# Kernel optimization log

Measured on AMD Instinct MI355X. Metric: run time of the kernel, lower is better.

Reference implementation:

```python
import jax, jax.numpy as jnp
import numpy as np

B, P, J, MOT, K, NB, WN, H = 64, 12273, 80, 94, 64, 20, 17, 128
W_POSE = 1.0

def euler_to_rotmat(a):
    # a: [..., 3] radians, R = Rz @ Ry @ Rx
    sx, sy, sz = jnp.sin(a[..., 0]), jnp.sin(a[..., 1]), jnp.sin(a[..., 2])
    cx, cy, cz = jnp.cos(a[..., 0]), jnp.cos(a[..., 1]), jnp.cos(a[..., 2])
    r00 = cz * cy; r01 = cz * sy * sx - sz * cx; r02 = cz * sy * cx + sz * sx
    r10 = sz * cy; r11 = sz * sy * sx + cz * cx; r12 = sz * sy * cx - cz * sx
    r20 = -sy;     r21 = cy * sx;                r22 = cy * cx
    return jnp.stack([jnp.stack([r00, r01, r02], -1),
                      jnp.stack([r10, r11, r12], -1),
                      jnp.stack([r20, r21, r22], -1)], -2)

def setup_inputs() -> dict:
    key = jax.random.key(0)
    ks = jax.random.split(key, 20)
    f32 = jnp.float32
    return {
        'in_pc_batch': jax.random.normal(ks[0], (B, P, 3), f32),
        't_nor': jax.random.normal(ks[1], (B, P, 3), f32),
        'rest_verts': jax.random.normal(ks[2], (P, 3), f32),
        'skin_weights': jax.random.uniform(ks[3], (P, J), f32),
        'mul_weight_list': jax.random.normal(ks[4], (J, MOT), f32),
        'query': jax.random.normal(ks[5], (B, J, 3), f32),
        'cloth_pose_std': jax.random.uniform(ks[6], (3,), f32),
        'cloth_pose_mean': jax.random.normal(ks[7], (3,), f32),
        'cloth_trans_std': jax.random.uniform(ks[8], (3,), f32),
        'cloth_trans_mean': jax.random.normal(ks[9], (3,), f32),
        'W1': jax.random.normal(ks[10], (3 + K, H), f32) * 0.1,
        'b1': jnp.zeros((H,), f32),
        'W2': jax.random.normal(ks[11], (H, 6), f32) * 0.1,
        'b2': jnp.zeros((6,), f32),
        'tmtemp': jax.random.normal(ks[12], (B, MOT, K), f32),
        'Wd': jax.random.normal(ks[13], (MOT * K, NB * WN), f32) * 0.02,
        'bd': jnp.zeros((NB * WN,), f32),
        'DPSD': jax.random.normal(ks[14], (NB, WN, P, 3), f32) * 0.1,
        'ssdr_res_std': jax.random.uniform(ks[15], (3,), f32),
        'ssdr_res_mean': jax.random.normal(ks[16], (3,), f32),
    }

def reference(in_pc_batch, t_nor, rest_verts, skin_weights, mul_weight_list,
              query, cloth_pose_std, cloth_pose_mean, cloth_trans_std,
              cloth_trans_mean, W1, b1, W2, b2, tmtemp, Wd, bd, DPSD,
              ssdr_res_std, ssdr_res_mean):
    # per-joint field input: [B, J, K]
    field_input = jnp.einsum('bjk,lj->blk', tmtemp, jax.nn.relu(mul_weight_list))
    # FieldNet: per-joint MLP on concat(query, field_input) -> [B, J, 6]
    h = jnp.concatenate([query, field_input], axis=-1)
    pred_rt = jax.nn.relu(h @ W1 + b1) @ W2 + b2
    pred_pose = pred_rt[..., 0:3] * cloth_pose_std + cloth_pose_mean
    pred_trans = (query + pred_rt[..., 3:6]) * cloth_trans_std + cloth_trans_mean
    # detailsnet + fused 20-basis accumulation: [B, P, 3]
    nbat = tmtemp.shape[0]
    detailkey = (tmtemp.reshape(nbat, -1) @ Wd + bd).reshape(nbat, NB, WN)
    detail_res = jnp.einsum('bnw,nwpx->bpx', detailkey, DPSD)
    detail_res = detail_res * ssdr_res_std + ssdr_res_mean
    # SSDR LBS skinning with Euler-angle rotations (degrees -> radians)
    R = euler_to_rotmat(jnp.deg2rad(pred_pose))            # [B, J, 3, 3]
    skinned = (jnp.einsum('pj,bjxy,py->bpx', skin_weights, R, rest_verts)
               + jnp.einsum('pj,bjx->bpx', skin_weights, pred_trans))
    out_pc = skinned + detail_res                          # [B, P, 3]
    loss_pose_l1 = jnp.mean(jnp.abs(in_pc_batch[:, :, 0:3] - out_pc))
    loss = loss_pose_l1 * W_POSE + 1e-4 * jnp.mean(DPSD ** 2)
    return loss[None], out_pc
```

## Files before the change

kernel.cpp:

```cpp
#include <hip/hip_runtime.h>

#define B_   64
#define P_   12273
#define J_   80
#define MOT_ 94
#define K_   64
#define H_   128
#define Q_   340
#define NE_  36819
#define MK_  6016
#define PW_  12288
#define STG_ 2356416

typedef float v4f  __attribute__((ext_vector_type(4)));
typedef float v8f  __attribute__((ext_vector_type(8)));
typedef float v16f __attribute__((ext_vector_type(16)));
#define AS4 __attribute__((address_space(4)))

__device__ __forceinline__ const AS4 float* unif(const float* p){
  return (const AS4 float*)(unsigned long long)p;
}
__device__ __forceinline__ const AS4 v4f* univ4(const float* p){
  return (const AS4 v4f*)(unsigned long long)p;
}
__device__ __forceinline__ const AS4 v16f* univ16(const float* p){
  return (const AS4 v16f*)(unsigned long long)p;
}

__global__ __launch_bounds__(256) void k_prep(
    const float* __restrict__ query, const float* __restrict__ mwl,
    const float* __restrict__ tm,    const float* __restrict__ W1,
    const float* __restrict__ b1,    const float* __restrict__ W2,
    const float* __restrict__ b2,    const float* __restrict__ cps,
    const float* __restrict__ cpm,   const float* __restrict__ cts,
    const float* __restrict__ ctm,   const float* __restrict__ skin,
    float* __restrict__ G,           float* __restrict__ tm_t,
    float* __restrict__ w_t,         float* __restrict__ lacc)
{
  __shared__ float smem[80 * 65];
  int blk = blockIdx.x;
  int t = threadIdx.x;
  if (blk < 1280){
    int lane = t & 63;
    int wid = __builtin_amdgcn_readfirstlane(t >> 6);
    int bj = blk * 4 + wid;
    int b = bj / J_, l = bj - b * J_;
    float* hs = smem + wid * 80;
    float acc = 0.f;
    const AS4 float* mp = unif(mwl + l * MOT_);
    const float* tp = tm + (size_t)b * MK_ + lane;
    float tbuf[4];
    #pragma unroll
    for (int s = 0; s < 4; s++) tbuf[s] = tp[s * K_];
    #pragma unroll 4
    for (int j = 0; j < MOT_; j++){
      float tv = tbuf[j & 3];
      if (j + 4 < MOT_) tbuf[j & 3] = tp[(j + 4) * K_];
      float w = mp[j]; w = w > 0.f ? w : 0.f;
      acc = fmaf(w, tv, acc);
    }
    hs[3 + lane] = acc;
    if (lane < 3) hs[lane] = query[(size_t)bj * 3 + lane];
    __syncthreads();
    float a1 = b1[lane], a2 = b1[lane + 64];
    float wa[4], wb[4];
    #pragma unroll
    for (int s = 0; s < 4; s++){
      wa[s] = W1[s * H_ + lane];
      wb[s] = W1[s * H_ + 64 + lane];
    }
    #pragma unroll 4
    for (int i = 0; i < 67; i++){
      float hv = hs[i];
      float va = wa[i & 3], vb = wb[i & 3];
      if (i + 4 < 67){
        wa[i & 3] = W1[(i + 4) * H_ + lane];
        wb[i & 3] = W1[(i + 4) * H_ + 64 + lane];
      }
      a1 = fmaf(hv, va, a1);
      a2 = fmaf(hv, vb, a2);
    }
    a1 = a1 > 0.f ? a1 : 0.f;
    a2 = a2 > 0.f ? a2 : 0.f;
    const AS4 float* b2c = unif(b2);
    float rt[6];
    #pragma unroll
    for (int o = 0; o < 6; o++){
      float po = fmaf(a1, W2[lane * 6 + o], a2 * W2[(lane + 64) * 6 + o]);
      #pragma unroll
      for (int off = 32; off; off >>= 1) po += __shfl_xor(po, off);
      rt[o] = po + b2c[o];
    }
    const float D2R = 0.017453292519943295f;
    float ax = fmaf(rt[0], cps[0], cpm[0]) * D2R;
    float ay = fmaf(rt[1], cps[1], cpm[1]) * D2R;
    float az = fmaf(rt[2], cps[2], cpm[2]) * D2R;
    float tx = fmaf(hs[0] + rt[3], cts[0], ctm[0]);
    float ty = fmaf(hs[1] + rt[4], cts[1], ctm[1]);
    float tz = fmaf(hs[2] + rt[5], cts[2], ctm[2]);
    float sx, cx, sy, cy, sz, cz;
    sincosf(ax, &sx, &cx); sincosf(ay, &sy, &cy); sincosf(az, &sz, &cz);
    if (lane == 0){
      float4 r0 = make_float4(cz*cy, cz*sy*sx - sz*cx, cz*sy*cx + sz*sx, tx);
      float4 r1 = make_float4(sz*cy, sz*sy*sx + cz*cx, sz*sy*cx - cz*sx, ty);
      float4 r2 = make_float4(-sy,   cy*sx,            cy*cx,            tz);
      float4* g = (float4*)(G + (size_t)bj * 12);
      g[0] = r0; g[1] = r1; g[2] = r2;
    }
  } else if (blk < 1374){
    int m0 = (blk - 1280) * 64;
    int ml = t & 63, g = t >> 6;
    #pragma unroll
    for (int r = 0; r < 16; r++){
      int b = g * 16 + r;
      smem[ml * 65 + b] = tm[(size_t)b * MK_ + m0 + ml];
    }
    __syncthreads();
    int bl = t & 63;
    #pragma unroll
    for (int r = 0; r < 16; r++){
      int m = g * 16 + r;
      tm_t[(size_t)(m0 + m) * 64 + bl] = smem[m * 65 + bl];
    }
  } else if (blk < 1566){
    int p0 = (blk - 1374) * 64;
    #pragma unroll
    for (int k = 0; k < 20; k++){
      int idx = k * 256 + t;
      int pl = idx / 80, j = idx - pl * 80;
      int p = p0 + pl;
      smem[j * 65 + pl] = (p < P_) ? skin[(size_t)p * J_ + j] : 0.f;
    }
    __syncthreads();
    #pragma unroll
    for (int k = 0; k < 20; k++){
      int idx = k * 256 + t;
      int j = idx >> 6, pl = idx & 63;
      w_t[(size_t)j * PW_ + p0 + pl] = smem[j * 65 + pl];
    }
  } else {
    if (t < 2) lacc[t] = 0.f;
  }
}

__global__ __launch_bounds__(256) void k_dkey(
    const float* __restrict__ tm_t, const float* __restrict__ Wd,
    float* __restrict__ part)
{
  int t = threadIdx.x;
  int lane = t & 63;
  int wid = __builtin_amdgcn_readfirstlane(t >> 6);
  int qt = blockIdx.x;
  int q = qt * 64 + lane;
  bool vq = q < Q_;
  int m0 = blockIdx.y * 64;
  const AS4 v16f* tr = univ16(tm_t);
  float acc[16];
  #pragma unroll
  for (int i = 0; i < 16; i++) acc[i] = 0.f;
  float wbuf[4];
  #pragma unroll
  for (int i = 0; i < 4; i++)
    wbuf[i] = vq ? Wd[(size_t)(m0 + i) * Q_ + q] : 0.f;
  v16f tb0 = tr[(size_t)(m0 + 0) * 4 + wid];
  v16f tb1 = tr[(size_t)(m0 + 1) * 4 + wid];
  #pragma unroll 4
  for (int mm = 0; mm < 60; mm++){
    float wd = wbuf[mm & 3];
    wbuf[mm & 3] = vq ? Wd[(size_t)(m0 + mm + 4) * Q_ + q] : 0.f;
    v16f tv = tb0; tb0 = tb1;
    tb1 = tr[(size_t)(m0 + mm + 2) * 4 + wid];
    #pragma unroll
    for (int i = 0; i < 16; i++) acc[i] = fmaf(tv[i], wd, acc[i]);
  }
  #pragma unroll
  for (int mm = 60; mm < 64; mm++){
    float wd = wbuf[mm & 3];
    v16f tv = tb0; tb0 = tb1;
    if (mm < 62) tb1 = tr[(size_t)(m0 + mm + 2) * 4 + wid];
    #pragma unroll
    for (int i = 0; i < 16; i++) acc[i] = fmaf(tv[i], wd, acc[i]);
  }
  float* pb = part + ((size_t)blockIdx.y * 6 + qt) * 4096 + (size_t)(wid * 16) * 64;
  #pragma unroll
  for (int i = 0; i < 16; i++) pb[i * 64 + lane] = acc[i];
}

__global__ __launch_bounds__(256) void k_dkred(
    const float* __restrict__ part, const float* __restrict__ bd,
    float* __restrict__ dk_t, int S)
{
  int t = threadIdx.x;
  int jj = blockIdx.x * 32 + (t >> 3);
  int dl = t & 7;
  int b = jj / Q_, q = jj - b * Q_;
  int qt = q >> 6, ql = q & 63;
  const float* pp = part + (size_t)qt * 4096 + b * 64 + ql;
  float s = 0.f;
  for (int d = dl; d < S; d += 8) s += pp[(size_t)d * 6 * 4096];
  s += __shfl_xor(s, 1); s += __shfl_xor(s, 2); s += __shfl_xor(s, 4);
  if (dl == 0) dk_t[q * 64 + b] = bd[q] + s;
}

__device__ __forceinline__ void dk_consume(const AS4 v16f* dkv, int qa, int wid,
                                           const float* dc, float* acc,
                                           float& sq, bool doSq)
{
  v16f r0 = dkv[(qa + 0) * 4 + wid];
  v16f r1 = dkv[(qa + 1) * 4 + wid];
  v16f r2 = dkv[(qa + 2) * 4 + wid];
  v16f r3 = dkv[(qa + 3) * 4 + wid];
  v16f r4 = dkv[(qa + 4) * 4 + wid];
  if (doSq){
    #pragma unroll
    for (int i = 0; i < 5; i++) sq = fmaf(dc[i], dc[i], sq);
  }
  #pragma unroll
  for (int i = 0; i < 16; i++){
    acc[i] = fmaf(r0[i], dc[0], acc[i]);
    acc[i] = fmaf(r1[i], dc[1], acc[i]);
    acc[i] = fmaf(r2[i], dc[2], acc[i]);
    acc[i] = fmaf(r3[i], dc[3], acc[i]);
    acc[i] = fmaf(r4[i], dc[4], acc[i]);
  }
}

__global__ __launch_bounds__(256) void k_detail(
    const float* __restrict__ DPSD, const float* __restrict__ dk_t,
    float* __restrict__ stg, float* __restrict__ out,
    float* __restrict__ lacc, int qn)
{
  int t = threadIdx.x;
  int lane = t & 63;
  int wid = __builtin_amdgcn_readfirstlane(t >> 6);
  int b0 = wid * 16;
  int e = blockIdx.x * 64 + lane;
  bool ve = e < NE_;
  int q0 = blockIdx.y * qn;
  const AS4 v16f* dkv = univ16(dk_t);
  const float* Dp = DPSD + (ve ? e : 0);
  float acc[16];
  #pragma unroll
  for (int i = 0; i < 16; i++) acc[i] = 0.f;
  float sq = 0.f;
  bool doSq = (wid == 0);
  int ng = qn / 5;
  float buf[4][5];
  #pragma unroll
  for (int s = 0; s < 4; s++){
    #pragma unroll
    for (int i = 0; i < 5; i++)
      buf[s][i] = Dp[(size_t)(q0 + s * 5 + i) * NE_];
  }
  for (int g = 0; g < ng; g += 4){
    #pragma unroll
    for (int s = 0; s < 4; s++){
      int gg = g + s;
      if (gg < ng){
        dk_consume(dkv, q0 + gg * 5, wid, buf[s], acc, sq, doSq);
        int gp = gg + 4;
        if (gp < ng){
          #pragma unroll
          for (int i = 0; i < 5; i++)
            buf[s][i] = Dp[(size_t)(q0 + gp * 5 + i) * NE_];
        }
      }
    }
  }
  if (ve){
    bool toOut = (blockIdx.y + 1 == gridDim.y);
    float* dst = toOut ? (out + 1 + e) : (stg + (size_t)blockIdx.y * STG_ + e);
    #pragma unroll
    for (int i = 0; i < 16; i++)
      dst[(size_t)(b0 + i) * NE_] = acc[i];
  }
  if (doSq){
    if (!ve) sq = 0.f;
    #pragma unroll
    for (int off = 32; off; off >>= 1) sq += __shfl_xor(sq, off);
    if (lane == 0) atomicAdd(&lacc[1], sq);
  }
}

__global__ __launch_bounds__(256) void k_skin(
    const float* __restrict__ G, const float* __restrict__ w_t,
    const float* __restrict__ rest, const float* __restrict__ in_pc,
    const float* __restrict__ stg, const float* __restrict__ rstd,
    const float* __restrict__ rmean,
    float* __restrict__ out, float* __restrict__ lacc, int nst)
{
  __shared__ float gs[7680];
  __shared__ float red[4];
  int t = threadIdx.x;
  int lane = t & 63;
  int wid = __builtin_amdgcn_readfirstlane(t >> 6);
  {
    const float4* Gv = (const float4*)(G + (size_t)blockIdx.y * 7680);
    float4* gv = (float4*)gs;
    #pragma unroll
    for (int it = 0; it < 8; it++){
      int idx = it * 256 + t;
      if (idx < 1920) gv[idx] = Gv[idx];
    }
  }
  __syncthreads();
  int p  = blockIdx.x * 64 + lane;
  int bA = blockIdx.y * 8 + wid * 2;
  const float4* gsA = (const float4*)(gs + (wid * 2) * 960);
  const float4* gsB = gsA + 240;
  float accA[12], accB[12];
  #pragma unroll
  for (int c = 0; c < 12; c++){ accA[c] = 0.f; accB[c] = 0.f; }
  const float* wp = w_t + p;
  float wbuf[8];
  #pragma unroll
  for (int s = 0; s < 8; s++) wbuf[s] = wp[(size_t)s * PW_];
  #pragma unroll 8
  for (int j = 0; j < J_; j++){
    float w = wbuf[j & 7];
    if (j + 8 < J_) wbuf[j & 7] = wp[(size_t)(j + 8) * PW_];
    float4 a0 = gsA[j * 3], a1 = gsA[j * 3 + 1], a2 = gsA[j * 3 + 2];
    float4 c0 = gsB[j * 3], c1 = gsB[j * 3 + 1], c2 = gsB[j * 3 + 2];
    accA[0]  = fmaf(w, a0.x, accA[0]);  accA[1]  = fmaf(w, a0.y, accA[1]);
    accA[2]  = fmaf(w, a0.z, accA[2]);  accA[3]  = fmaf(w, a0.w, accA[3]);
    accA[4]  = fmaf(w, a1.x, accA[4]);  accA[5]  = fmaf(w, a1.y, accA[5]);
    accA[6]  = fmaf(w, a1.z, accA[6]);  accA[7]  = fmaf(w, a1.w, accA[7]);
    accA[8]  = fmaf(w, a2.x, accA[8]);  accA[9]  = fmaf(w, a2.y, accA[9]);
    accA[10] = fmaf(w, a2.z, accA[10]); accA[11] = fmaf(w, a2.w, accA[11]);
    accB[0]  = fmaf(w, c0.x, accB[0]);  accB[1]  = fmaf(w, c0.y, accB[1]);
    accB[2]  = fmaf(w, c0.z, accB[2]);  accB[3]  = fmaf(w, c0.w, accB[3]);
    accB[4]  = fmaf(w, c1.x, accB[4]);  accB[5]  = fmaf(w, c1.y, accB[5]);
    accB[6]  = fmaf(w, c1.z, accB[6]);  accB[7]  = fmaf(w, c1.w, accB[7]);
    accB[8]  = fmaf(w, c2.x, accB[8]);  accB[9]  = fmaf(w, c2.y, accB[9]);
    accB[10] = fmaf(w, c2.z, accB[10]); accB[11] = fmaf(w, c2.w, accB[11]);
  }
  bool vp = p < P_;
  float vx = 0.f, vy = 0.f, vz = 0.f;
  if (vp){ vx = rest[p * 3]; vy = rest[p * 3 + 1]; vz = rest[p * 3 + 2]; }
  float srs[3], srm[3];
  #pragma unroll
  for (int x = 0; x < 3; x++){ srs[x] = rstd[x]; srm[x] = rmean[x]; }
  float lsum = 0.f;
  if (vp){
    size_t baseA = ((size_t)bA * P_ + p) * 3;
    size_t baseB = baseA + (size_t)P_ * 3;
    #pragma unroll
    for (int x = 0; x < 3; x++){
      float det = out[1 + baseA + x];
      for (int s = 0; s < nst; s++) det += stg[(size_t)s * STG_ + baseA + x];
      float v = fmaf(accA[x*4+0], vx, fmaf(accA[x*4+1], vy, fmaf(accA[x*4+2], vz, accA[x*4+3])));
      v += fmaf(det, srs[x], srm[x]);
      lsum += fabsf(in_pc[baseA + x] - v);
      out[1 + baseA + x] = v;
    }
    #pragma unroll
    for (int x = 0; x < 3; x++){
      float det = out[1 + baseB + x];
      for (int s = 0; s < nst; s++) det += stg[(size_t)s * STG_ + baseB + x];
      float v = fmaf(accB[x*4+0], vx, fmaf(accB[x*4+1], vy, fmaf(accB[x*4+2], vz, accB[x*4+3])));
      v += fmaf(det, srs[x], srm[x]);
      lsum += fabsf(in_pc[baseB + x] - v);
      out[1 + baseB + x] = v;
    }
  }
  #pragma unroll
  for (int off = 32; off; off >>= 1) lsum += __shfl_xor(lsum, off);
  if (lane == 0) red[wid] = lsum;
  __syncthreads();
  if (t == 0) atomicAdd(&lacc[0], red[0] + red[1] + red[2] + red[3]);
}

__global__ void k_finalize(const float* __restrict__ lacc, float* __restrict__ out){
  if (threadIdx.x == 0 && blockIdx.x == 0){
    float loss = lacc[0] * (1.f / 2356416.f) + 1e-4f * (lacc[1] * (1.f / 12518460.f));
    out[0] = loss;
  }
}

extern "C" void kernel_launch(void* const* d_in, const int* in_sizes, int n_in,
                              void* d_out, int out_size, void* d_ws, size_t ws_size,
                              hipStream_t stream){
  const float* in_pc = (const float*)d_in[0];
  const float* rest  = (const float*)d_in[2];
  const float* skin  = (const float*)d_in[3];
  const float* mwl   = (const float*)d_in[4];
  const float* query = (const float*)d_in[5];
  const float* cps   = (const float*)d_in[6];
  const float* cpm   = (const float*)d_in[7];
  const float* cts   = (const float*)d_in[8];
  const float* ctm   = (const float*)d_in[9];
  const float* W1    = (const float*)d_in[10];
  const float* b1    = (const float*)d_in[11];
  const float* W2    = (const float*)d_in[12];
  const float* b2    = (const float*)d_in[13];
  const float* tm    = (const float*)d_in[14];
  const float* Wd    = (const float*)d_in[15];
  const float* bd    = (const float*)d_in[16];
  const float* DPSD  = (const float*)d_in[17];
  const float* rstd  = (const float*)d_in[18];
  const float* rmean = (const float*)d_in[19];
  float* out = (float*)d_out;

  float* ws   = (float*)d_ws;
  float* G    = ws;
  float* dk_t = G + 61440;
  float* lacc = dk_t + 21760;
  float* tm_t = lacc + 64;
  float* w_t  = tm_t + 385024;
  float* un   = w_t + 983040;

  size_t have = ws_size / 4;
  int nqh = (have >= (size_t)(1451328 + 2356416)) ? 2 : 1;
  int qn = Q_ / nqh;

  k_prep    <<<1567, 256, 0, stream>>>(query, mwl, tm, W1, b1, W2, b2,
                                       cps, cpm, cts, ctm, skin,
                                       G, tm_t, w_t, lacc);
  k_dkey    <<<dim3(6, 94), 256, 0, stream>>>(tm_t, Wd, un);
  k_dkred   <<<680, 256, 0, stream>>>(un, bd, dk_t, 94);
  k_detail  <<<dim3(576, nqh), 256, 0, stream>>>(DPSD, dk_t, un, out, lacc, qn);
  k_skin    <<<dim3(192, 8), 256, 0, stream>>>(G, w_t, rest, in_pc, un, rstd, rmean,
                                               out, lacc, nqh - 1);
  k_finalize<<<1, 64, 0, stream>>>(lacc, out);
}
```

Before: 310.3 us.

## Retile detail GEMV with LDS double-buffered DPSD and rework skin kernel

```diff
diff --git a/kernel.cpp b/kernel.cpp
--- a/kernel.cpp
+++ b/kernel.cpp
@@ -13,7 +13,6 @@
 #define STG_ 2356416
 
 typedef float v4f  __attribute__((ext_vector_type(4)));
-typedef float v8f  __attribute__((ext_vector_type(8)));
 typedef float v16f __attribute__((ext_vector_type(16)));
 #define AS4 __attribute__((address_space(4)))
 
@@ -202,84 +201,125 @@
   if (dl == 0) dk_t[q * 64 + b] = bd[q] + s;
 }
 
-__device__ __forceinline__ void dk_consume(const AS4 v16f* dkv, int qa, int wid,
-                                           const float* dc, float* acc,
-                                           float& sq, bool doSq)
-{
-  v16f r0 = dkv[(qa + 0) * 4 + wid];
-  v16f r1 = dkv[(qa + 1) * 4 + wid];
-  v16f r2 = dkv[(qa + 2) * 4 + wid];
-  v16f r3 = dkv[(qa + 3) * 4 + wid];
-  v16f r4 = dkv[(qa + 4) * 4 + wid];
+template<bool TAIL>
+__device__ __forceinline__ void cons_q(const v16f& dk, const v4f& d,
+                                       v4f* acc, float& sq, bool doSq, int e4)
+{
   if (doSq){
     #pragma unroll
-    for (int i = 0; i < 5; i++) sq = fmaf(dc[i], dc[i], sq);
+    for (int c = 0; c < 4; c++)
+      if (!TAIL || (e4 + c) < NE_) sq = fmaf(d[c], d[c], sq);
   }
   #pragma unroll
   for (int i = 0; i < 16; i++){
-    acc[i] = fmaf(r0[i], dc[0], acc[i]);
-    acc[i] = fmaf(r1[i], dc[1], acc[i]);
-    acc[i] = fmaf(r2[i], dc[2], acc[i]);
-    acc[i] = fmaf(r3[i], dc[3], acc[i]);
-    acc[i] = fmaf(r4[i], dc[4], acc[i]);
-  }
-}
-
-__global__ __launch_bounds__(256) void k_detail(
+    #pragma unroll
+    for (int c = 0; c < 4; c++)
+      acc[i][c] = fmaf(dk[i], d[c], acc[i][c]);
+  }
+}
+
+template<bool TAIL>
+__device__ __forceinline__ void detail_body(
     const float* __restrict__ DPSD, const float* __restrict__ dk_t,
     float* __restrict__ stg, float* __restrict__ out,
-    float* __restrict__ lacc, int qn)
+    float* __restrict__ lacc, int QSTEP, float* sbuf)
 {
   int t = threadIdx.x;
   int lane = t & 63;
   int wid = __builtin_amdgcn_readfirstlane(t >> 6);
   int b0 = wid * 16;
-  int e = blockIdx.x * 64 + lane;
-  bool ve = e < NE_;
-  int q0 = blockIdx.y * qn;
-  const AS4 v16f* dkv = univ16(dk_t);
-  const float* Dp = DPSD + (ve ? e : 0);
-  float acc[16];
-  #pragma unroll
-  for (int i = 0; i < 16; i++) acc[i] = 0.f;
+  int e4 = blockIdx.x * 256 + lane * 4;
+  int q0 = blockIdx.y * QSTEP;
+  int qn = min(QSTEP, Q_ - q0);
+  int nt = qn >> 2;
+  const AS4 v16f* tr = univ16(dk_t);
+  bool doSq = (wid == 0);
+  v4f acc[16];
+  #pragma unroll
+  for (int i = 0; i < 16; i++){
+    #pragma unroll
+    for (int c = 0; c < 4; c++) acc[i][c] = 0.f;
+  }
   float sq = 0.f;
-  bool doSq = (wid == 0);
-  int ng = qn / 5;
-  float buf[4][5];
-  #pragma unroll
-  for (int s = 0; s < 4; s++){
-    #pragma unroll
-    for (int i = 0; i < 5; i++)
-      buf[s][i] = Dp[(size_t)(q0 + s * 5 + i) * NE_];
-  }
-  for (int g = 0; g < ng; g += 4){
-    #pragma unroll
-    for (int s = 0; s < 4; s++){
-      int gg = g + s;
-      if (gg < ng){
-        dk_consume(dkv, q0 + gg * 5, wid, buf[s], acc, sq, doSq);
-        int gp = gg + 4;
-        if (gp < ng){
-          #pragma unroll
-          for (int i = 0; i < 5; i++)
-            buf[s][i] = Dp[(size_t)(q0 + gp * 5 + i) * NE_];
-        }
+  float nx0, nx1, nx2, nx3;
+  {
+    size_t base = (size_t)(q0 + wid) * NE_;
+    int ea = e4, eb = e4 + 1, ec = e4 + 2, ed = e4 + 3;
+    if (TAIL){
+      ea = ea < NE_ ? ea : NE_ - 1; eb = eb < NE_ ? eb : NE_ - 1;
+      ec = ec < NE_ ? ec : NE_ - 1; ed = ed < NE_ ? ed : NE_ - 1;
+    }
+    nx0 = DPSD[base + ea]; nx1 = DPSD[base + eb];
+    nx2 = DPSD[base + ec]; nx3 = DPSD[base + ed];
+    v4f vv = {nx0, nx1, nx2, nx3};
+    *(v4f*)(sbuf + wid * 256 + lane * 4) = vv;
+  }
+  __syncthreads();
+  v16f dkA0 = tr[(size_t)(q0 + 0) * 4 + wid];
+  v16f dkA1 = tr[(size_t)(q0 + 1) * 4 + wid];
+  int cur = 0;
+  for (int tt = 0; tt < nt; tt++){
+    int qb = q0 + tt * 4;
+    bool more = (tt + 1 < nt);
+    if (more){
+      size_t base = (size_t)(qb + 4 + wid) * NE_;
+      int ea = e4, eb = e4 + 1, ec = e4 + 2, ed = e4 + 3;
+      if (TAIL){
+        ea = ea < NE_ ? ea : NE_ - 1; eb = eb < NE_ ? eb : NE_ - 1;
+        ec = ec < NE_ ? ec : NE_ - 1; ed = ed < NE_ ? ed : NE_ - 1;
       }
-    }
-  }
-  if (ve){
-    bool toOut = (blockIdx.y + 1 == gridDim.y);
-    float* dst = toOut ? (out + 1 + e) : (stg + (size_t)blockIdx.y * STG_ + e);
-    #pragma unroll
-    for (int i = 0; i < 16; i++)
-      dst[(size_t)(b0 + i) * NE_] = acc[i];
+      nx0 = DPSD[base + ea]; nx1 = DPSD[base + eb];
+      nx2 = DPSD[base + ec]; nx3 = DPSD[base + ed];
+    }
+    const float* sb = sbuf + cur * 1024;
+    v16f dkB0 = tr[(size_t)(qb + 2) * 4 + wid];
+    v16f dkB1 = tr[(size_t)(qb + 3) * 4 + wid];
+    v4f d0 = *(const v4f*)(sb + 0 * 256 + lane * 4);
+    v4f d1 = *(const v4f*)(sb + 1 * 256 + lane * 4);
+    cons_q<TAIL>(dkA0, d0, acc, sq, doSq, e4);
+    cons_q<TAIL>(dkA1, d1, acc, sq, doSq, e4);
+    int qnx = min(qb + 4, Q_ - 2);
+    dkA0 = tr[(size_t)(qnx + 0) * 4 + wid];
+    dkA1 = tr[(size_t)(qnx + 1) * 4 + wid];
+    v4f d2 = *(const v4f*)(sb + 2 * 256 + lane * 4);
+    v4f d3 = *(const v4f*)(sb + 3 * 256 + lane * 4);
+    cons_q<TAIL>(dkB0, d2, acc, sq, doSq, e4);
+    cons_q<TAIL>(dkB1, d3, acc, sq, doSq, e4);
+    if (more){
+      v4f vv = {nx0, nx1, nx2, nx3};
+      *(v4f*)(sbuf + (cur ^ 1) * 1024 + wid * 256 + lane * 4) = vv;
+    }
+    __syncthreads();
+    cur ^= 1;
+  }
+  bool toOut = (blockIdx.y + 1 == gridDim.y);
+  float* dst = toOut ? (out + 1) : (stg + (size_t)blockIdx.y * STG_);
+  #pragma unroll
+  for (int i = 0; i < 16; i++){
+    size_t rb = (size_t)(b0 + i) * NE_;
+    #pragma unroll
+    for (int c = 0; c < 4; c++){
+      int e = e4 + c;
+      if (!TAIL || e < NE_) dst[rb + e] = acc[i][c];
+    }
   }
   if (doSq){
-    if (!ve) sq = 0.f;
     #pragma unroll
     for (int off = 32; off; off >>= 1) sq += __shfl_xor(sq, off);
     if (lane == 0) atomicAdd(&lacc[1], sq);
   }
+}
+
+__global__ __launch_bounds__(256) void k_detail(
+    const float* __restrict__ DPSD, const float* __restrict__ dk_t,
+    float* __restrict__ stg, float* __restrict__ out,
+    float* __restrict__ lacc, int QSTEP)
+{
+  __shared__ float sbuf[2048];
+  if (blockIdx.x == gridDim.x - 1)
+    detail_body<true>(DPSD, dk_t, stg, out, lacc, QSTEP, sbuf);
+  else
+    detail_body<false>(DPSD, dk_t, stg, out, lacc, QSTEP, sbuf);
 }
 
 __global__ __launch_bounds__(256) void k_skin(
@@ -289,59 +329,49 @@
     const float* __restrict__ rmean,
     float* __restrict__ out, float* __restrict__ lacc, int nst)
 {
-  __shared__ float gs[7680];
-  __shared__ float red[4];
   int t = threadIdx.x;
   int lane = t & 63;
   int wid = __builtin_amdgcn_readfirstlane(t >> 6);
-  {
-    const float4* Gv = (const float4*)(G + (size_t)blockIdx.y * 7680);
-    float4* gv = (float4*)gs;
-    #pragma unroll
-    for (int it = 0; it < 8; it++){
-      int idx = it * 256 + t;
-      if (idx < 1920) gv[idx] = Gv[idx];
-    }
-  }
-  __syncthreads();
-  int p  = blockIdx.x * 64 + lane;
-  int bA = blockIdx.y * 8 + wid * 2;
-  const float4* gsA = (const float4*)(gs + (wid * 2) * 960);
-  const float4* gsB = gsA + 240;
+  int p = blockIdx.x * 256 + wid * 64 + lane;
+  int bA = blockIdx.y * 2;
+  const AS4 v4f* gA = univ4(G + (size_t)bA * J_ * 12);
+  const AS4 v4f* gB = univ4(G + ((size_t)bA + 1) * J_ * 12);
   float accA[12], accB[12];
   #pragma unroll
   for (int c = 0; c < 12; c++){ accA[c] = 0.f; accB[c] = 0.f; }
   const float* wp = w_t + p;
-  float wbuf[8];
-  #pragma unroll
-  for (int s = 0; s < 8; s++) wbuf[s] = wp[(size_t)s * PW_];
-  #pragma unroll 8
+  v4f A0[2], A1[2], A2[2], B0[2], B1[2], B2[2];
+  A0[0] = gA[0]; A1[0] = gA[1]; A2[0] = gA[2];
+  B0[0] = gB[0]; B1[0] = gB[1]; B2[0] = gB[2];
+  #pragma unroll 2
   for (int j = 0; j < J_; j++){
-    float w = wbuf[j & 7];
-    if (j + 8 < J_) wbuf[j & 7] = wp[(size_t)(j + 8) * PW_];
-    float4 a0 = gsA[j * 3], a1 = gsA[j * 3 + 1], a2 = gsA[j * 3 + 2];
-    float4 c0 = gsB[j * 3], c1 = gsB[j * 3 + 1], c2 = gsB[j * 3 + 2];
-    accA[0]  = fmaf(w, a0.x, accA[0]);  accA[1]  = fmaf(w, a0.y, accA[1]);
-    accA[2]  = fmaf(w, a0.z, accA[2]);  accA[3]  = fmaf(w, a0.w, accA[3]);
-    accA[4]  = fmaf(w, a1.x, accA[4]);  accA[5]  = fmaf(w, a1.y, accA[5]);
-    accA[6]  = fmaf(w, a1.z, accA[6]);  accA[7]  = fmaf(w, a1.w, accA[7]);
-    accA[8]  = fmaf(w, a2.x, accA[8]);  accA[9]  = fmaf(w, a2.y, accA[9]);
-    accA[10] = fmaf(w, a2.z, accA[10]); accA[11] = fmaf(w, a2.w, accA[11]);
-    accB[0]  = fmaf(w, c0.x, accB[0]);  accB[1]  = fmaf(w, c0.y, accB[1]);
-    accB[2]  = fmaf(w, c0.z, accB[2]);  accB[3]  = fmaf(w, c0.w, accB[3]);
-    accB[4]  = fmaf(w, c1.x, accB[4]);  accB[5]  = fmaf(w, c1.y, accB[5]);
-    accB[6]  = fmaf(w, c1.z, accB[6]);  accB[7]  = fmaf(w, c1.w, accB[7]);
-    accB[8]  = fmaf(w, c2.x, accB[8]);  accB[9]  = fmaf(w, c2.y, accB[9]);
-    accB[10] = fmaf(w, c2.z, accB[10]); accB[11] = fmaf(w, c2.w, accB[11]);
-  }
-  bool vp = p < P_;
-  float vx = 0.f, vy = 0.f, vz = 0.f;
-  if (vp){ vx = rest[p * 3]; vy = rest[p * 3 + 1]; vz = rest[p * 3 + 2]; }
+    int cs = j & 1, ns = cs ^ 1;
+    if (j + 1 < J_){
+      A0[ns] = gA[(j + 1) * 3 + 0];
+      A1[ns] = gA[(j + 1) * 3 + 1];
+      A2[ns] = gA[(j + 1) * 3 + 2];
+      B0[ns] = gB[(j + 1) * 3 + 0];
+      B1[ns] = gB[(j + 1) * 3 + 1];
+      B2[ns] = gB[(j + 1) * 3 + 2];
+    }
+    float w = wp[(size_t)j * PW_];
+    #pragma unroll
+    for (int c = 0; c < 4; c++){
+      accA[c]     = fmaf(w, A0[cs][c], accA[c]);
+      accA[4 + c] = fmaf(w, A1[cs][c], accA[4 + c]);
+      accA[8 + c] = fmaf(w, A2[cs][c], accA[8 + c]);
+      accB[c]     = fmaf(w, B0[cs][c], accB[c]);
+      accB[4 + c] = fmaf(w, B1[cs][c], accB[4 + c]);
+      accB[8 + c] = fmaf(w, B2[cs][c], accB[8 + c]);
+    }
+  }
   float srs[3], srm[3];
   #pragma unroll
   for (int x = 0; x < 3; x++){ srs[x] = rstd[x]; srm[x] = rmean[x]; }
   float lsum = 0.f;
+  bool vp = p < P_;
   if (vp){
+    float vx = rest[p * 3], vy = rest[p * 3 + 1], vz = rest[p * 3 + 2];
     size_t baseA = ((size_t)bA * P_ + p) * 3;
     size_t baseB = baseA + (size_t)P_ * 3;
     #pragma unroll
@@ -365,6 +395,7 @@
   }
   #pragma unroll
   for (int off = 32; off; off >>= 1) lsum += __shfl_xor(lsum, off);
+  __shared__ float red[4];
   if (lane == 0) red[wid] = lsum;
   __syncthreads();
   if (t == 0) atomicAdd(&lacc[0], red[0] + red[1] + red[2] + red[3]);
@@ -410,16 +441,19 @@
   float* un   = w_t + 983040;
 
   size_t have = ws_size / 4;
-  int nqh = (have >= (size_t)(1451328 + 2356416)) ? 2 : 1;
-  int qn = Q_ / nqh;
+  const size_t base = 1451328;
+  int nqh, QSTEP;
+  if (have >= base + 3 * (size_t)STG_)      { nqh = 4; QSTEP = 88;  }
+  else if (have >= base + (size_t)STG_)     { nqh = 2; QSTEP = 172; }
+  else                                      { nqh = 1; QSTEP = 340; }
 
   k_prep    <<<1567, 256, 0, stream>>>(query, mwl, tm, W1, b1, W2, b2,
                                        cps, cpm, cts, ctm, skin,
                                        G, tm_t, w_t, lacc);
   k_dkey    <<<dim3(6, 94), 256, 0, stream>>>(tm_t, Wd, un);
   k_dkred   <<<680, 256, 0, stream>>>(un, bd, dk_t, 94);
-  k_detail  <<<dim3(576, nqh), 256, 0, stream>>>(DPSD, dk_t, un, out, lacc, qn);
-  k_skin    <<<dim3(192, 8), 256, 0, stream>>>(G, w_t, rest, in_pc, un, rstd, rmean,
+  k_detail  <<<dim3(144, nqh), 256, 0, stream>>>(DPSD, dk_t, un, out, lacc, QSTEP);
+  k_skin    <<<dim3(48, 32), 256, 0, stream>>>(G, w_t, rest, in_pc, un, rstd, rmean,
                                                out, lacc, nqh - 1);
   k_finalize<<<1, 64, 0, stream>>>(lacc, out);
 }
```

New measurement: 289.5 us. 6.7% less time.
